# Kernel tuning notes

Hardware: AMD Instinct MI355X
Metric: run time of the kernel (lower is better)

The kernel has to match this reference:

```python
import jax, jax.numpy as jnp
import numpy as np

B, C, H, W = 8, 64, 64, 64


def setup_inputs() -> dict:
    key = jax.random.key(0)
    ks = jax.random.split(key, 8)
    s = 1.0 / np.sqrt(C)  # keep logits in a reasonable range
    return {
        "x": jax.random.normal(ks[0], (B, C, H, W), dtype=jnp.float32),
        "Wf": jax.random.normal(ks[1], (C, C), dtype=jnp.float32) * s,
        "bf": jax.random.normal(ks[2], (C,), dtype=jnp.float32) * s,
        "Wg": jax.random.normal(ks[3], (C, C), dtype=jnp.float32) * s,
        "bg": jax.random.normal(ks[4], (C,), dtype=jnp.float32) * s,
        "Wh": jax.random.normal(ks[5], (C, C), dtype=jnp.float32) * s,
        "bh": jax.random.normal(ks[6], (C,), dtype=jnp.float32) * s,
        "gamma": jax.random.normal(ks[7], (1,), dtype=jnp.float32),
    }


def reference(x, Wf, bf, Wg, bg, Wh, bh, gamma):
    b, c, h, w = x.shape
    n = h * w
    xf = x.reshape(b, c, n)  # [B, C, N]
    # 1x1 convs == per-pixel channel GEMMs
    f = jnp.einsum("oc,bcn->bon", Wf, xf) + bf[None, :, None]  # [B, C, N]
    g = jnp.einsum("oc,bcn->bon", Wg, xf) + bg[None, :, None]
    hh = jnp.einsum("oc,bcn->bon", Wh, xf) + bh[None, :, None]
    # att_in[b, i, j] = f[b, :, i] . g[b, :, j]  (f_x permuted then bmm with g_x)
    att = jax.nn.softmax(jnp.einsum("bci,bcj->bij", f, g), axis=-1)  # [B, N, N]
    # torch.bmm(h_x, attention): out[b, c, j] = sum_i h[b, c, i] * att[b, i, j]
    out = jnp.einsum("bci,bij->bcj", hh, att).reshape(b, c, h, w)
    return gamma[0] * out + x
```

## Files before the change

### kernel.cpp

```cpp
#include <hip/hip_runtime.h>

#define BB 8
#define CC 64
#define NN 4096
#define JCH 8
#define LOG2E 1.4426950408889634f

typedef float f32x4  __attribute__((ext_vector_type(4)));
typedef float f32x16 __attribute__((ext_vector_type(16)));
typedef _Float16 half8_t __attribute__((ext_vector_type(8)));
typedef int int4v __attribute__((ext_vector_type(4)));
typedef unsigned uint2v __attribute__((ext_vector_type(2)));


__global__ __launch_bounds__(384, 6) void qkv_kernel(
    const float* __restrict__ x,
    const float* __restrict__ Wf, const float* __restrict__ bf,
    const float* __restrict__ Wg, const float* __restrict__ bg,
    const float* __restrict__ Wh, const float* __restrict__ bh,
    _Float16* __restrict__ fT, _Float16* __restrict__ gT,
    _Float16* __restrict__ hT)
{
    __shared__ float xbuf[64][36];

    const int tid  = threadIdx.x;
    const int lane = tid & 63;
    const int wv   = tid >> 6;
    const int l31  = lane & 31;
    const int q5   = lane >> 5;
    const int z    = wv >> 1;
    const int ot   = wv & 1;
    const int n0   = blockIdx.x * 32;
    const int b    = blockIdx.y;

    if (tid < 256) {
        const int row = tid >> 2;
        const int px4 = (tid & 3) * 8;
        const float* src = x + (size_t)(b * CC + row) * NN + n0 + px4;
        *(f32x4*)&xbuf[row][px4]     = *(const f32x4*)(src);
        *(f32x4*)&xbuf[row][px4 + 4] = *(const f32x4*)(src + 4);
    }
    __syncthreads();

    half8_t xf[4];
#pragma unroll
    for (int kc = 0; kc < 4; ++kc) {
        const int kb = kc * 16 + q5 * 8;
        int4v p;
#pragma unroll
        for (int h2 = 0; h2 < 4; ++h2) {
            p[h2] = __builtin_bit_cast(int, __builtin_amdgcn_cvt_pkrtz(
                xbuf[kb + h2 * 2][l31], xbuf[kb + h2 * 2 + 1][l31]));
        }
        xf[kc] = __builtin_bit_cast(half8_t, p);
    }

    const float* W    = (z == 0) ? Wf : ((z == 1) ? Wg : Wh);
    const float* bias = (z == 0) ? bf : ((z == 1) ? bg : bh);

    half8_t wf[4];
    {
        const float* wrow = W + (size_t)(ot * 32 + l31) * CC;
#pragma unroll
        for (int kc = 0; kc < 4; ++kc) {
            const f32x4 w0 = *(const f32x4*)(wrow + kc * 16 + q5 * 8);
            const f32x4 w1 = *(const f32x4*)(wrow + kc * 16 + q5 * 8 + 4);
            int4v p;
            p[0] = __builtin_bit_cast(int, __builtin_amdgcn_cvt_pkrtz(w0[0], w0[1]));
            p[1] = __builtin_bit_cast(int, __builtin_amdgcn_cvt_pkrtz(w0[2], w0[3]));
            p[2] = __builtin_bit_cast(int, __builtin_amdgcn_cvt_pkrtz(w1[0], w1[1]));
            p[3] = __builtin_bit_cast(int, __builtin_amdgcn_cvt_pkrtz(w1[2], w1[3]));
            wf[kc] = __builtin_bit_cast(half8_t, p);
        }
    }

    if (z < 2) {
        f32x16 acc = {};
#pragma unroll
        for (int kc = 0; kc < 4; ++kc)
            acc = __builtin_amdgcn_mfma_f32_32x32x16_f16(xf[kc], wf[kc], acc, 0, 0, 0);
        _Float16* dstT = (z == 0) ? fT : gT;
        const float scale = (z == 0) ? LOG2E : 1.0f;
        const float bv = bias[ot * 32 + l31];
#pragma unroll
        for (int r = 0; r < 16; ++r) {
            const int prow = (r & 3) + 8 * (r >> 2) + 4 * q5;
            dstT[(size_t)(b * NN + n0 + prow) * CC + ot * 32 + l31] =
                (_Float16)((acc[r] + bv) * scale);
        }
    } else {
        f32x16 acc = {};
#pragma unroll
        for (int kc = 0; kc < 4; ++kc)
            acc = __builtin_amdgcn_mfma_f32_32x32x16_f16(wf[kc], xf[kc], acc, 0, 0, 0);
        _Float16* hbase = hT + ((size_t)(b * (NN / 32) + blockIdx.x) * CC) * 32;
#pragma unroll
        for (int rb = 0; rb < 4; ++rb) {
            const f32x4 b4 = *(const f32x4*)(bias + ot * 32 + rb * 8 + q5 * 4);
#pragma unroll
            for (int k = 0; k < 4; ++k) {
                const int c = ot * 32 + rb * 8 + q5 * 4 + k;
                hbase[(size_t)c * 32 + l31] = (_Float16)(acc[rb * 4 + k] + b4[k]);
            }
        }
    }
}

__global__ __launch_bounds__(256, 4) void stats_kernel(
    const _Float16* __restrict__ fT, const _Float16* __restrict__ gT,
    float* __restrict__ lpart)
{
    __shared__ _Float16 gbuf[2][64][72];

    const int lane = threadIdx.x & 63;
    const int wv   = threadIdx.x >> 6;
    const int b    = blockIdx.y;
    const int jc   = blockIdx.z;
    const int i0   = blockIdx.x * 128 + wv * 32;
    const int l31  = lane & 31;
    const int q5   = lane >> 5;

    half8_t a[4];
    const _Float16* fa = fT + (size_t)(b * NN + i0 + l31) * CC + q5 * 8;
#pragma unroll
    for (int kc = 0; kc < 4; ++kc) a[kc] = *(const half8_t*)(fa + kc * 16);

    const _Float16* gchunk = gT + (size_t)(b * NN + jc * (NN / JCH)) * CC;
    const int T = NN / JCH / 64;

    const int srow = wv * 16 + (lane >> 3);
    const int scol = (lane & 7) * 8;

    {
        const half8_t v0 = *(const half8_t*)(gchunk + (size_t)srow * CC + scol);
        const half8_t v1 = *(const half8_t*)(gchunk + (size_t)(srow + 8) * CC + scol);
        *(half8_t*)&gbuf[0][srow][scol] = v0;
        *(half8_t*)&gbuf[0][srow + 8][scol] = v1;
    }
    __syncthreads();

    float l16[16];
#pragma unroll
    for (int r = 0; r < 16; ++r) l16[r] = 0.f;

    for (int t = 0; t < T; ++t) {
        const int buf = t & 1;
        const bool pf = (t + 1 < T);
        half8_t p0, p1;
        if (pf) {
            const _Float16* src = gchunk + (size_t)((t + 1) * 64 + srow) * CC + scol;
            p0 = *(const half8_t*)(src);
            p1 = *(const half8_t*)(src + 8 * CC);
        }
#pragma unroll
        for (int js = 0; js < 2; ++js) {
            const _Float16* grow = &gbuf[buf][js * 32 + l31][0] + q5 * 8;
            f32x16 s = {};
#pragma unroll
            for (int kc = 0; kc < 4; ++kc) {
                const half8_t bfr = *(const half8_t*)(grow + kc * 16);
                s = __builtin_amdgcn_mfma_f32_32x32x16_f16(a[kc], bfr, s, 0, 0, 0);
            }
#pragma unroll
            for (int r = 0; r < 16; ++r) l16[r] += __builtin_exp2f(s[r]);
        }
        if (pf) {
            *(half8_t*)&gbuf[buf ^ 1][srow][scol] = p0;
            *(half8_t*)&gbuf[buf ^ 1][srow + 8][scol] = p1;
        }
        __syncthreads();
    }

#pragma unroll
    for (int r = 0; r < 16; ++r) {
#pragma unroll
        for (int off = 1; off < 32; off <<= 1)
            l16[r] += __shfl_xor(l16[r], off);
    }

    if (l31 == 0) {
        float* lp = lpart + (size_t)jc * BB * NN + b * NN + i0;
#pragma unroll
        for (int rb = 0; rb < 4; ++rb) {
            f32x4 v;
#pragma unroll
            for (int k = 0; k < 4; ++k) v[k] = l16[rb * 4 + k];
            *(f32x4*)(lp + rb * 8 + q5 * 4) = v;
        }
    }
}

template <int NICT>
__global__ __launch_bounds__(256, 2) void attn_kernel(
    const _Float16* __restrict__ fT, const _Float16* __restrict__ gT,
    const _Float16* __restrict__ hT, const float* __restrict__ lpart,
    _Float16* __restrict__ pout)
{
    constexpr int ichunk = NN / NICT;
    __shared__ _Float16 fbuf[2][64][72];
    __shared__ _Float16 hbuf[2][64][72];
    __shared__ float nbbuf[ichunk];

    const int lane = threadIdx.x & 63;
    const int wv   = threadIdx.x >> 6;
    const int b    = blockIdx.y;
    const int ic   = blockIdx.z;
    const int l31  = lane & 31;
    const int q5   = lane >> 5;
    const int jbase = blockIdx.x * 256 + wv * 64;

    const int ibase  = ic * ichunk;
    const int tid    = threadIdx.x;

    if (tid * 4 < ichunk) {
        const float* lp0 = lpart + b * NN + ibase + tid * 4;
        f32x4 sum = *(const f32x4*)(lp0);
#pragma unroll
        for (int jc = 1; jc < JCH; ++jc) {
            const f32x4 v = *(const f32x4*)(lp0 + (size_t)jc * BB * NN);
#pragma unroll
            for (int k = 0; k < 4; ++k) sum[k] += v[k];
        }
        f32x4 nb4;
#pragma unroll
        for (int k = 0; k < 4; ++k) nb4[k] = -__builtin_log2f(sum[k]);
        *(f32x4*)&nbbuf[tid * 4] = nb4;
    }

    half8_t bg[2][4];
#pragma unroll
    for (int jt = 0; jt < 2; ++jt) {
        const _Float16* grow = gT + (size_t)(b * NN + jbase + jt * 32 + l31) * CC + q5 * 8;
#pragma unroll
        for (int kc = 0; kc < 4; ++kc) bg[jt][kc] = *(const half8_t*)(grow + kc * 16);
    }

    f32x16 acc[2][2] = {};

    const _Float16* fchunk = fT + ((size_t)b * NN + ibase) * CC;
    const _Float16* hchunk = hT + ((size_t)(b * (NN / 32) + ibase / 32) * CC) * 32;
    const int T = ichunk / 64;

    const int frow_s = tid >> 2;
    const int fcol_s = (tid & 3) * 16;
    const int hrow_s = tid >> 2;
    const int hcol_s = (tid & 3) * 8;

    {
        const half8_t f0 = *(const half8_t*)(fchunk + (size_t)frow_s * CC + fcol_s);
        const half8_t f1 = *(const half8_t*)(fchunk + (size_t)frow_s * CC + fcol_s + 8);
        const half8_t h0 = *(const half8_t*)(hchunk + tid * 8);
        const half8_t h1 = *(const half8_t*)(hchunk + 2048 + tid * 8);
        *(half8_t*)&fbuf[0][frow_s][fcol_s]     = f0;
        *(half8_t*)&fbuf[0][frow_s][fcol_s + 8] = f1;
        *(half8_t*)&hbuf[0][hrow_s][hcol_s]      = h0;
        *(half8_t*)&hbuf[0][hrow_s][32 + hcol_s] = h1;
    }
    __syncthreads();

    for (int t = 0; t < T; ++t) {
        const int buf = t & 1;
        const bool pf = (t + 1 < T);
        half8_t pf0, pf1, ph0, ph1;
        if (pf) {
            const _Float16* fsrc = fchunk + (size_t)((t + 1) * 64 + frow_s) * CC + fcol_s;
            const _Float16* hsrc = hchunk + (size_t)(t + 1) * 4096 + tid * 8;
            pf0 = *(const half8_t*)(fsrc);
            pf1 = *(const half8_t*)(fsrc + 8);
            ph0 = *(const half8_t*)(hsrc);
            ph1 = *(const half8_t*)(hsrc + 2048);
        }

#pragma unroll
        for (int ih = 0; ih < 2; ++ih) {
            f32x16 s0;
#pragma unroll
            for (int rb = 0; rb < 4; ++rb) {
                const f32x4 n4 = *(const f32x4*)&nbbuf[t * 64 + ih * 32 + rb * 8 + q5 * 4];
#pragma unroll
                for (int k = 0; k < 4; ++k) s0[rb * 4 + k] = n4[k];
            }
            f32x16 s1 = s0;
            const _Float16* frow = &fbuf[buf][ih * 32 + l31][0] + q5 * 8;
#pragma unroll
            for (int kc = 0; kc < 4; ++kc) {
                const half8_t af = *(const half8_t*)(frow + kc * 16);
                s0 = __builtin_amdgcn_mfma_f32_32x32x16_f16(af, bg[0][kc], s0, 0, 0, 0);
                s1 = __builtin_amdgcn_mfma_f32_32x32x16_f16(af, bg[1][kc], s1, 0, 0, 0);
            }

            half8_t B[2][2];
#pragma unroll
            for (int jt = 0; jt < 2; ++jt) {
                const f32x16& s = jt ? s1 : s0;
                int e[8];
#pragma unroll
                for (int r8 = 0; r8 < 8; ++r8) {
                    e[r8] = __builtin_bit_cast(int, __builtin_amdgcn_cvt_pkrtz(
                        __builtin_exp2f(s[r8 * 2]), __builtin_exp2f(s[r8 * 2 + 1])));
                }
                int4v b0, b1;
#if __has_builtin(__builtin_amdgcn_permlane32_swap)
                const uint2v p02 = __builtin_amdgcn_permlane32_swap(
                    (unsigned)e[0], (unsigned)e[2], false, false);
                const uint2v p13 = __builtin_amdgcn_permlane32_swap(
                    (unsigned)e[1], (unsigned)e[3], false, false);
                const uint2v p46 = __builtin_amdgcn_permlane32_swap(
                    (unsigned)e[4], (unsigned)e[6], false, false);
                const uint2v p57 = __builtin_amdgcn_permlane32_swap(
                    (unsigned)e[5], (unsigned)e[7], false, false);
                b0[0] = (int)p02[0]; b0[1] = (int)p13[0];
                b0[2] = (int)p02[1]; b0[3] = (int)p13[1];
                b1[0] = (int)p46[0]; b1[1] = (int)p57[0];
                b1[2] = (int)p46[1]; b1[3] = (int)p57[1];
#else
                const int sA = q5 ? e[0] : e[2];
                const int sB = q5 ? e[1] : e[3];
                const int sC = q5 ? e[4] : e[6];
                const int sD = q5 ? e[5] : e[7];
                const int rA = __shfl_xor(sA, 32, 64);
                const int rB = __shfl_xor(sB, 32, 64);
                const int rC = __shfl_xor(sC, 32, 64);
                const int rD = __shfl_xor(sD, 32, 64);
                b0[0] = q5 ? rA   : e[0];
                b0[1] = q5 ? rB   : e[1];
                b0[2] = q5 ? e[2] : rA;
                b0[3] = q5 ? e[3] : rB;
                b1[0] = q5 ? rC   : e[4];
                b1[1] = q5 ? rD   : e[5];
                b1[2] = q5 ? e[6] : rC;
                b1[3] = q5 ? e[7] : rD;
#endif
                B[jt][0] = __builtin_bit_cast(half8_t, b0);
                B[jt][1] = __builtin_bit_cast(half8_t, b1);
            }

#pragma unroll
            for (int ct = 0; ct < 2; ++ct) {
                const half8_t ah0 = *(const half8_t*)(&hbuf[buf][ct * 32 + l31][0] + ih * 32 + q5 * 8);
                const half8_t ah1 = *(const half8_t*)(&hbuf[buf][ct * 32 + l31][0] + ih * 32 + 16 + q5 * 8);
                acc[0][ct] = __builtin_amdgcn_mfma_f32_32x32x16_f16(ah0, B[0][0], acc[0][ct], 0, 0, 0);
                acc[0][ct] = __builtin_amdgcn_mfma_f32_32x32x16_f16(ah1, B[0][1], acc[0][ct], 0, 0, 0);
                acc[1][ct] = __builtin_amdgcn_mfma_f32_32x32x16_f16(ah0, B[1][0], acc[1][ct], 0, 0, 0);
                acc[1][ct] = __builtin_amdgcn_mfma_f32_32x32x16_f16(ah1, B[1][1], acc[1][ct], 0, 0, 0);
            }
        }

        if (pf) {
            *(half8_t*)&fbuf[buf ^ 1][frow_s][fcol_s]     = pf0;
            *(half8_t*)&fbuf[buf ^ 1][frow_s][fcol_s + 8] = pf1;
            *(half8_t*)&hbuf[buf ^ 1][hrow_s][hcol_s]      = ph0;
            *(half8_t*)&hbuf[buf ^ 1][hrow_s][32 + hcol_s] = ph1;
        }
        __syncthreads();
    }

    _Float16* pb_out = pout + (((size_t)ic * BB + b) * CC) * NN;
#pragma unroll
    for (int jt = 0; jt < 2; ++jt) {
        const int j = jbase + jt * 32 + l31;
#pragma unroll
        for (int ct = 0; ct < 2; ++ct) {
#pragma unroll
            for (int r = 0; r < 16; ++r) {
                const int c = ct * 32 + (r & 3) + 8 * (r >> 2) + 4 * q5;
                pb_out[(size_t)c * NN + j] = (_Float16)acc[jt][ct][r];
            }
        }
    }
}

template <int NICT>
__global__ __launch_bounds__(256) void combine_kernel(
    const float* __restrict__ x, const float* __restrict__ gammap,
    const _Float16* __restrict__ pout, float* __restrict__ out)
{
    const float gam = gammap[0];
    const size_t i8 = ((size_t)blockIdx.x * 256 + threadIdx.x) * 8;
    const size_t TOT = (size_t)BB * CC * NN;

    float s[8] = {0.f, 0.f, 0.f, 0.f, 0.f, 0.f, 0.f, 0.f};
#pragma unroll
    for (int ic = 0; ic < NICT; ++ic) {
        const half8_t p = *(const half8_t*)(pout + ic * TOT + i8);
#pragma unroll
        for (int k = 0; k < 8; ++k) s[k] += (float)p[k];
    }
    const f32x4 x0 = *(const f32x4*)(x + i8);
    const f32x4 x1 = *(const f32x4*)(x + i8 + 4);
    f32x4 o0, o1;
#pragma unroll
    for (int k = 0; k < 4; ++k) { o0[k] = gam * s[k] + x0[k]; o1[k] = gam * s[k + 4] + x1[k]; }
    *(f32x4*)(out + i8) = o0;
    *(f32x4*)(out + i8 + 4) = o1;
}

extern "C" void kernel_launch(void* const* d_in, const int* in_sizes, int n_in,
                              void* d_out, int out_size, void* d_ws, size_t ws_size,
                              hipStream_t stream) {
    const float* x     = (const float*)d_in[0];
    const float* Wf    = (const float*)d_in[1];
    const float* bf    = (const float*)d_in[2];
    const float* Wg    = (const float*)d_in[3];
    const float* bg    = (const float*)d_in[4];
    const float* Wh    = (const float*)d_in[5];
    const float* bh    = (const float*)d_in[6];
    const float* gamma = (const float*)d_in[7];
    float* out = (float*)d_out;

    const size_t TOT = (size_t)BB * CC * NN;
    _Float16* fT   = (_Float16*)d_ws;
    _Float16* gT   = fT + TOT;
    _Float16* hT   = gT + TOT;
    _Float16* pout = hT + TOT;
    float* lpart   = (float*)(pout + (size_t)4 * TOT);

    qkv_kernel<<<dim3(NN / 32, BB), 384, 0, stream>>>(
        x, Wf, bf, Wg, bg, Wh, bh, fT, gT, hT);
    stats_kernel<<<dim3(NN / 128, BB, JCH), 256, 0, stream>>>(fT, gT, lpart);
    attn_kernel<4><<<dim3(NN / 256, BB, 4), 256, 0, stream>>>(fT, gT, hT, lpart, pout);
    combine_kernel<4><<<dim3(TOT / (256 * 8)), 256, 0, stream>>>(x, gamma, pout, out);
}
```

Measured before the change: 168.2 us.

## Load f and h operands directly from global into registers, drop LDS staging

The attention kernel no longer stages f and h tiles through double-buffered shared memory with per-iteration barriers. Each wave now loads its MFMA operand fragments straight from global memory (L2/L1), with a register prefetch of the next f tile and per-iteration h loads. This removes LDS traffic and the __syncthreads in the main loop and frees shared memory for occupancy. In exchange, the four waves of a block redundantly fetch the same f/h data from global, raising cache traffic and register pressure, and the h loads are not prefetched ahead.

After: 177.2 us. 5.3% more time.

```diff
diff --git a/kernel.cpp b/kernel.cpp
--- a/kernel.cpp
+++ b/kernel.cpp
@@ -197,8 +197,6 @@
     _Float16* __restrict__ pout)
 {
     constexpr int ichunk = NN / NICT;
-    __shared__ _Float16 fbuf[2][64][72];
-    __shared__ _Float16 hbuf[2][64][72];
     __shared__ float nbbuf[ichunk];
 
     const int lane = threadIdx.x & 63;
@@ -235,41 +233,43 @@
         for (int kc = 0; kc < 4; ++kc) bg[jt][kc] = *(const half8_t*)(grow + kc * 16);
     }
 
+    __syncthreads();
+
     f32x16 acc[2][2] = {};
 
     const _Float16* fchunk = fT + ((size_t)b * NN + ibase) * CC;
     const _Float16* hchunk = hT + ((size_t)(b * (NN / 32) + ibase / 32) * CC) * 32;
     const int T = ichunk / 64;
 
-    const int frow_s = tid >> 2;
-    const int fcol_s = (tid & 3) * 16;
-    const int hrow_s = tid >> 2;
-    const int hcol_s = (tid & 3) * 8;
-
-    {
-        const half8_t f0 = *(const half8_t*)(fchunk + (size_t)frow_s * CC + fcol_s);
-        const half8_t f1 = *(const half8_t*)(fchunk + (size_t)frow_s * CC + fcol_s + 8);
-        const half8_t h0 = *(const half8_t*)(hchunk + tid * 8);
-        const half8_t h1 = *(const half8_t*)(hchunk + 2048 + tid * 8);
-        *(half8_t*)&fbuf[0][frow_s][fcol_s]     = f0;
-        *(half8_t*)&fbuf[0][frow_s][fcol_s + 8] = f1;
-        *(half8_t*)&hbuf[0][hrow_s][hcol_s]      = h0;
-        *(half8_t*)&hbuf[0][hrow_s][32 + hcol_s] = h1;
-    }
-    __syncthreads();
+    const _Float16* fw = fchunk + (size_t)l31 * CC + q5 * 8;
+    const _Float16* hw = hchunk + (size_t)l31 * 32 + q5 * 8;
+
+    half8_t fc[2][4];
+#pragma unroll
+    for (int ih = 0; ih < 2; ++ih)
+#pragma unroll
+        for (int kc = 0; kc < 4; ++kc)
+            fc[ih][kc] = *(const half8_t*)(fw + (size_t)(ih * 32) * CC + kc * 16);
 
     for (int t = 0; t < T; ++t) {
-        const int buf = t & 1;
+        half8_t fn[2][4];
         const bool pf = (t + 1 < T);
-        half8_t pf0, pf1, ph0, ph1;
         if (pf) {
-            const _Float16* fsrc = fchunk + (size_t)((t + 1) * 64 + frow_s) * CC + fcol_s;
-            const _Float16* hsrc = hchunk + (size_t)(t + 1) * 4096 + tid * 8;
-            pf0 = *(const half8_t*)(fsrc);
-            pf1 = *(const half8_t*)(fsrc + 8);
-            ph0 = *(const half8_t*)(hsrc);
-            ph1 = *(const half8_t*)(hsrc + 2048);
-        }
+#pragma unroll
+            for (int ih = 0; ih < 2; ++ih)
+#pragma unroll
+                for (int kc = 0; kc < 4; ++kc)
+                    fn[ih][kc] = *(const half8_t*)(fw + (size_t)((t + 1) * 64 + ih * 32) * CC + kc * 16);
+        }
+        half8_t ah[2][2][2];
+#pragma unroll
+        for (int ih = 0; ih < 2; ++ih)
+#pragma unroll
+            for (int ct = 0; ct < 2; ++ct) {
+                const _Float16* hb = hw + (size_t)(t * 2 + ih) * 2048 + ct * 1024;
+                ah[ih][ct][0] = *(const half8_t*)(hb);
+                ah[ih][ct][1] = *(const half8_t*)(hb + 16);
+            }
 
 #pragma unroll
         for (int ih = 0; ih < 2; ++ih) {
@@ -281,10 +281,9 @@
                 for (int k = 0; k < 4; ++k) s0[rb * 4 + k] = n4[k];
             }
             f32x16 s1 = s0;
-            const _Float16* frow = &fbuf[buf][ih * 32 + l31][0] + q5 * 8;
 #pragma unroll
             for (int kc = 0; kc < 4; ++kc) {
-                const half8_t af = *(const half8_t*)(frow + kc * 16);
+                const half8_t af = fc[ih][kc];
                 s0 = __builtin_amdgcn_mfma_f32_32x32x16_f16(af, bg[0][kc], s0, 0, 0, 0);
                 s1 = __builtin_amdgcn_mfma_f32_32x32x16_f16(af, bg[1][kc], s1, 0, 0, 0);
             }
@@ -337,8 +336,8 @@
 
 #pragma unroll
             for (int ct = 0; ct < 2; ++ct) {
-                const half8_t ah0 = *(const half8_t*)(&hbuf[buf][ct * 32 + l31][0] + ih * 32 + q5 * 8);
-                const half8_t ah1 = *(const half8_t*)(&hbuf[buf][ct * 32 + l31][0] + ih * 32 + 16 + q5 * 8);
+                const half8_t ah0 = ah[ih][ct][0];
+                const half8_t ah1 = ah[ih][ct][1];
                 acc[0][ct] = __builtin_amdgcn_mfma_f32_32x32x16_f16(ah0, B[0][0], acc[0][ct], 0, 0, 0);
                 acc[0][ct] = __builtin_amdgcn_mfma_f32_32x32x16_f16(ah1, B[0][1], acc[0][ct], 0, 0, 0);
                 acc[1][ct] = __builtin_amdgcn_mfma_f32_32x32x16_f16(ah0, B[1][0], acc[1][ct], 0, 0, 0);
@@ -347,12 +346,12 @@
         }
 
         if (pf) {
-            *(half8_t*)&fbuf[buf ^ 1][frow_s][fcol_s]     = pf0;
-            *(half8_t*)&fbuf[buf ^ 1][frow_s][fcol_s + 8] = pf1;
-            *(half8_t*)&hbuf[buf ^ 1][hrow_s][hcol_s]      = ph0;
-            *(half8_t*)&hbuf[buf ^ 1][hrow_s][32 + hcol_s] = ph1;
-        }
-        __syncthreads();
+#pragma unroll
+            for (int ih = 0; ih < 2; ++ih)
+#pragma unroll
+                for (int kc = 0; kc < 4; ++kc)
+                    fc[ih][kc] = fn[ih][kc];
+        }
     }
 
     _Float16* pb_out = pout + (((size_t)ic * BB + b) * CC) * NN;
```
